# Kernel optimization log

Measured on AMD Instinct MI355X. Metric: run time of the kernel, lower is better.

Reference implementation:

```python
import jax, jax.numpy as jnp
import numpy as np

B, S, H, U = 32, 4096, 512, 512


def setup_inputs() -> dict:
    key = jax.random.key(0)
    ks = jax.random.split(key, 6)
    scale = 1.0 / np.sqrt(H)
    return {
        "query": jax.random.normal(ks[0], (B, H), dtype=jnp.float32),
        "values": jax.random.normal(ks[1], (B, S, H), dtype=jnp.float32),
        "W1": jax.random.normal(ks[2], (H, U), dtype=jnp.float32) * scale,
        "b1": jnp.zeros((U,), dtype=jnp.float32),
        "W2": jax.random.normal(ks[3], (H, U), dtype=jnp.float32) * scale,
        "b2": jnp.zeros((U,), dtype=jnp.float32),
        "va": jax.random.normal(ks[4], (U, 1), dtype=jnp.float32) * (1.0 / np.sqrt(U)),
        "bva": jnp.zeros((1,), dtype=jnp.float32),
    }


def reference(query, values, W1, b1, W2, b2, va, bva):
    # query: [B, H] -> [B, 1, U]; values: [B, S, H] -> [B, S, U]
    q_proj = jnp.einsum('bh,hu->bu', query, W1) + b1           # [B, U]
    v_proj = jnp.einsum('bsh,hu->bsu', values, W2) + b2        # [B, S, U]
    scores = jnp.einsum('bsu,uo->bso', jnp.tanh(q_proj[:, None, :] + v_proj), va) + bva  # [B, S, 1]
    attention_weights = jax.nn.softmax(scores, axis=1)         # [B, S, 1]
    context_vector = jnp.sum(attention_weights * values, axis=1)  # [B, H]
    return attention_weights, context_vector
```

## Files before the change

kernel.cpp:

```cpp
#include <hip/hip_runtime.h>
#include <hip/hip_bf16.h>
#include <stdint.h>

#define B_SZ 32
#define S_SZ 4096
#define H_SZ 512
#define U_SZ 512

typedef __attribute__((ext_vector_type(8)))  _Float16 half8;
typedef __attribute__((ext_vector_type(4)))  _Float16 half4_t;
typedef __attribute__((ext_vector_type(16))) float    floatx16;

__global__ __launch_bounds__(256) void qproj_kernel(
    const float* __restrict__ query, const float* __restrict__ W1,
    const float* __restrict__ b1, const float* __restrict__ b2,
    float* __restrict__ qpb2)
{
    const int b = blockIdx.x;
    const int u = blockIdx.y * 256 + threadIdx.x;
    float acc = b1[u] + b2[u];
    const float* q = query + b * H_SZ;
    for (int h = 0; h < H_SZ; ++h)
        acc += q[h] * W1[h * U_SZ + u];
    qpb2[b * U_SZ + u] = acc;
}

__global__ __launch_bounds__(256) void w2swizzle_kernel(
    const float* __restrict__ W2, _Float16* __restrict__ W2s)
{
    const int i = blockIdx.x * 256 + threadIdx.x;
    const int k = i >> 9;
    const int n = i & 511;
    const int idx = (k >> 4) * 8192 + ((k >> 3) & 1) * 4096 + n * 8 + (k & 7);
    W2s[idx] = (_Float16)W2[i];
}

__global__ __launch_bounds__(256, 2) void scores_kernel(
    const float* __restrict__ values, const _Float16* __restrict__ W2s,
    const float* __restrict__ qpb2, const float* __restrict__ va,
    const float* __restrict__ bva, float* __restrict__ scores)
{
    __shared__ __align__(16) _Float16 A_lds[1024];
    __shared__ __align__(16) _Float16 B_lds[8192];
    __shared__ float sc[64 * 33];

    const int t    = threadIdx.x;
    const int lane = t & 63;
    const int w    = t >> 6;
    const int l31  = lane & 31;
    const int kh   = lane >> 5;
    const int m0   = blockIdx.x * 64;
    const int b    = m0 >> 12;

    const float* Arow = values + (size_t)m0 * H_SZ;

    floatx16 acc[2][4];
#pragma unroll
    for (int s = 0; s < 2; ++s)
#pragma unroll
        for (int nt = 0; nt < 4; ++nt) acc[s][nt] = (floatx16)(0.0f);

    const int sm = t >> 2;
    const int kq = t & 3;
    const int aw = ((kq >> 1) * 64 + sm) * 8 + (kq & 1) * 4;

    const uint4* Wsrc = reinterpret_cast<const uint4*>(W2s);
    uint4* Bl4 = reinterpret_cast<uint4*>(B_lds);

    for (int kb = 0; kb < 32; ++kb) {
        __syncthreads();
        float4 av = *reinterpret_cast<const float4*>(Arow + sm * H_SZ + kb * 16 + kq * 4);
        half4_t ah;
        ah.x = (_Float16)av.x; ah.y = (_Float16)av.y;
        ah.z = (_Float16)av.z; ah.w = (_Float16)av.w;
        *reinterpret_cast<half4_t*>(&A_lds[aw]) = ah;
#pragma unroll
        for (int i = 0; i < 4; ++i)
            Bl4[t * 4 + i] = Wsrc[kb * 1024 + t * 4 + i];
        __syncthreads();

        half8 a0 = *reinterpret_cast<const half8*>(&A_lds[kh * 512 + l31 * 8]);
        half8 a1 = *reinterpret_cast<const half8*>(&A_lds[kh * 512 + 256 + l31 * 8]);
#pragma unroll
        for (int nt = 0; nt < 4; ++nt) {
            half8 bf = *reinterpret_cast<const half8*>(
                &B_lds[kh * 4096 + ((w * 4 + nt) * 32 + l31) * 8]);
            acc[0][nt] = __builtin_amdgcn_mfma_f32_32x32x16_f16(a0, bf, acc[0][nt], 0, 0, 0);
            acc[1][nt] = __builtin_amdgcn_mfma_f32_32x32x16_f16(a1, bf, acc[1][nt], 0, 0, 0);
        }
    }

    float qv[4], vv[4];
#pragma unroll
    for (int nt = 0; nt < 4; ++nt) {
        int n = w * 128 + nt * 32 + l31;
        qv[nt] = qpb2[b * U_SZ + n];
        vv[nt] = va[n];
    }
    __syncthreads();
    for (int i = t; i < 64 * 33; i += 256) sc[i] = 0.0f;
    __syncthreads();
#pragma unroll
    for (int s = 0; s < 2; ++s) {
#pragma unroll
        for (int r = 0; r < 16; ++r) {
            float p = 0.0f;
#pragma unroll
            for (int nt = 0; nt < 4; ++nt) {
                float x = acc[s][nt][r] + qv[nt];
                float e = __expf(2.0f * x);
                p += (1.0f - 2.0f / (e + 1.0f)) * vv[nt];
            }
            int ml = s * 32 + (r & 3) + 8 * (r >> 2) + 4 * kh;
            atomicAdd(&sc[ml * 33 + l31], p);
        }
    }
    __syncthreads();
    if (t < 64) {
        float sum = *bva;
#pragma unroll
        for (int c = 0; c < 32; ++c) sum += sc[t * 33 + c];
        scores[m0 + t] = sum;
    }
}

__global__ __launch_bounds__(1024) void softmax_kernel(
    const float* __restrict__ scores, float* __restrict__ out)
{
    __shared__ float red[16];
    __shared__ float s_max, s_sum;
    const int b = blockIdx.x;
    const int t = threadIdx.x;

    float4 v = *reinterpret_cast<const float4*>(scores + b * S_SZ + t * 4);
    float m = fmaxf(fmaxf(v.x, v.y), fmaxf(v.z, v.w));
#pragma unroll
    for (int o = 32; o > 0; o >>= 1) m = fmaxf(m, __shfl_xor(m, o));
    if ((t & 63) == 0) red[t >> 6] = m;
    __syncthreads();
    if (t == 0) {
        float mm = red[0];
        for (int i = 1; i < 16; ++i) mm = fmaxf(mm, red[i]);
        s_max = mm;
    }
    __syncthreads();
    float mm = s_max;
    float4 e;
    e.x = __expf(v.x - mm); e.y = __expf(v.y - mm);
    e.z = __expf(v.z - mm); e.w = __expf(v.w - mm);
    float s = e.x + e.y + e.z + e.w;
#pragma unroll
    for (int o = 32; o > 0; o >>= 1) s += __shfl_xor(s, o);
    if ((t & 63) == 0) red[t >> 6] = s;
    __syncthreads();
    if (t == 0) {
        float ss = 0.0f;
        for (int i = 0; i < 16; ++i) ss += red[i];
        s_sum = ss;
    }
    __syncthreads();
    float rinv = 1.0f / s_sum;
    float4 wv;
    wv.x = e.x * rinv; wv.y = e.y * rinv; wv.z = e.z * rinv; wv.w = e.w * rinv;
    *reinterpret_cast<float4*>(out + b * S_SZ + t * 4) = wv;

    if (t < 512) out[B_SZ * S_SZ + b * 512 + t] = 0.0f;
}

__global__ __launch_bounds__(256) void context_kernel(
    const float* __restrict__ values, const float* __restrict__ wts,
    float* __restrict__ ctx)
{
    __shared__ float wl[512];
    __shared__ __align__(16) float part[4][64][4];
    const int ss = blockIdx.x;
    const int hc = blockIdx.y;
    const int b  = blockIdx.z;
    const int t  = threadIdx.x;
    const int l = t & 63, g = t >> 6;

    if (t < 128)
        *reinterpret_cast<float4*>(&wl[t * 4]) =
            *reinterpret_cast<const float4*>(wts + b * S_SZ + ss * 512 + t * 4);
    __syncthreads();

    const int h = hc * 256 + l * 4;
    const float* vp = values + ((size_t)(b * S_SZ + ss * 512 + g * 128)) * H_SZ + h;
    float4 a = {0.f, 0.f, 0.f, 0.f};
    for (int i = 0; i < 128; ++i) {
        float wv = wl[g * 128 + i];
        float4 v = *reinterpret_cast<const float4*>(vp + (size_t)i * H_SZ);
        a.x += wv * v.x; a.y += wv * v.y; a.z += wv * v.z; a.w += wv * v.w;
    }
    *reinterpret_cast<float4*>(&part[g][l][0]) = a;
    __syncthreads();
    if (t < 64) {
        float4 sacc = *reinterpret_cast<float4*>(&part[0][t][0]);
#pragma unroll
        for (int gg = 1; gg < 4; ++gg) {
            float4 p = *reinterpret_cast<float4*>(&part[gg][t][0]);
            sacc.x += p.x; sacc.y += p.y; sacc.z += p.z; sacc.w += p.w;
        }
        int hh = hc * 256 + t * 4;
        atomicAdd(&ctx[b * H_SZ + hh + 0], sacc.x);
        atomicAdd(&ctx[b * H_SZ + hh + 1], sacc.y);
        atomicAdd(&ctx[b * H_SZ + hh + 2], sacc.z);
        atomicAdd(&ctx[b * H_SZ + hh + 3], sacc.w);
    }
}

extern "C" void kernel_launch(void* const* d_in, const int* in_sizes, int n_in,
                              void* d_out, int out_size, void* d_ws, size_t ws_size,
                              hipStream_t stream) {
    const float* query  = (const float*)d_in[0];
    const float* values = (const float*)d_in[1];
    const float* W1     = (const float*)d_in[2];
    const float* b1     = (const float*)d_in[3];
    const float* W2     = (const float*)d_in[4];
    const float* b2     = (const float*)d_in[5];
    const float* va     = (const float*)d_in[6];
    const float* bva    = (const float*)d_in[7];
    float* out = (float*)d_out;

    char* ws = (char*)d_ws;
    float*    qpb2   = (float*)ws;
    _Float16* W2s    = (_Float16*)(ws + 65536);
    float*    scores = (float*)(ws + 65536 + 524288);

    qproj_kernel<<<dim3(32, 2), 256, 0, stream>>>(query, W1, b1, b2, qpb2);
    w2swizzle_kernel<<<1024, 256, 0, stream>>>(W2, W2s);
    scores_kernel<<<2048, 256, 0, stream>>>(values, W2s, qpb2, va, bva, scores);
    softmax_kernel<<<32, 1024, 0, stream>>>(scores, out);
    context_kernel<<<dim3(8, 2, 32), 256, 0, stream>>>(values, out, out + B_SZ * S_SZ);
}
```

Baseline: 577.8 us.

## Rewrite scores GEMM with async double-buffered LDS and fuse softmax into context

```diff
diff --git a/kernel.cpp b/kernel.cpp
--- a/kernel.cpp
+++ b/kernel.cpp
@@ -7,32 +7,42 @@
 #define H_SZ 512
 #define U_SZ 512
 
-typedef __attribute__((ext_vector_type(8)))  _Float16 half8;
-typedef __attribute__((ext_vector_type(4)))  _Float16 half4_t;
-typedef __attribute__((ext_vector_type(16))) float    floatx16;
+typedef __attribute__((ext_vector_type(8))) _Float16 half8;
+typedef __attribute__((ext_vector_type(4))) float floatx4;
+
+__device__ __forceinline__ void async_copy16(const void* g, void* l) {
+    __builtin_amdgcn_global_load_lds(
+        (const __attribute__((address_space(1))) void*)g,
+        (__attribute__((address_space(3))) void*)l, 16, 0, 0);
+}
+
+__global__ __launch_bounds__(256) void prep_kernel(
+    const float* __restrict__ W2, _Float16* __restrict__ W2s,
+    float* __restrict__ qpb2, float* __restrict__ ctx)
+{
+    const int t = threadIdx.x;
+    const int bid = blockIdx.x;
+    const int i = bid * 256 + t;
+    const int k = i >> 9, n = i & 511;
+    W2s[(k >> 5) * 16384 + ((k >> 3) & 3) * 4096 + n * 8 + (k & 7)] =
+        (_Float16)W2[i];
+    if (bid < 64) qpb2[i] = 0.0f;
+    else if (bid < 128) ctx[(bid - 64) * 256 + t] = 0.0f;
+}
 
 __global__ __launch_bounds__(256) void qproj_kernel(
     const float* __restrict__ query, const float* __restrict__ W1,
     const float* __restrict__ b1, const float* __restrict__ b2,
     float* __restrict__ qpb2)
 {
-    const int b = blockIdx.x;
-    const int u = blockIdx.y * 256 + threadIdx.x;
-    float acc = b1[u] + b2[u];
-    const float* q = query + b * H_SZ;
-    for (int h = 0; h < H_SZ; ++h)
-        acc += q[h] * W1[h * U_SZ + u];
-    qpb2[b * U_SZ + u] = acc;
-}
-
-__global__ __launch_bounds__(256) void w2swizzle_kernel(
-    const float* __restrict__ W2, _Float16* __restrict__ W2s)
-{
-    const int i = blockIdx.x * 256 + threadIdx.x;
-    const int k = i >> 9;
-    const int n = i & 511;
-    const int idx = (k >> 4) * 8192 + ((k >> 3) & 1) * 4096 + n * 8 + (k & 7);
-    W2s[idx] = (_Float16)W2[i];
+    const int b = blockIdx.x, uc = blockIdx.y, ks = blockIdx.z;
+    const int u = uc * 256 + threadIdx.x;
+    float acc = (ks == 0) ? (b1[u] + b2[u]) : 0.0f;
+    const float* q  = query + b * H_SZ + ks * 128;
+    const float* Wp = W1 + (size_t)(ks * 128) * U_SZ + u;
+    for (int k = 0; k < 128; ++k)
+        acc = fmaf(q[k], Wp[(size_t)k * U_SZ], acc);
+    atomicAdd(&qpb2[b * U_SZ + u], acc);
 }
 
 __global__ __launch_bounds__(256, 2) void scores_kernel(
@@ -40,99 +50,125 @@
     const float* __restrict__ qpb2, const float* __restrict__ va,
     const float* __restrict__ bva, float* __restrict__ scores)
 {
-    __shared__ __align__(16) _Float16 A_lds[1024];
-    __shared__ __align__(16) _Float16 B_lds[8192];
-    __shared__ float sc[64 * 33];
-
-    const int t    = threadIdx.x;
-    const int lane = t & 63;
-    const int w    = t >> 6;
-    const int l31  = lane & 31;
-    const int kh   = lane >> 5;
-    const int m0   = blockIdx.x * 64;
-    const int b    = m0 >> 12;
-
-    const float* Arow = values + (size_t)m0 * H_SZ;
-
-    floatx16 acc[2][4];
-#pragma unroll
-    for (int s = 0; s < 2; ++s)
-#pragma unroll
-        for (int nt = 0; nt < 4; ++nt) acc[s][nt] = (floatx16)(0.0f);
-
-    const int sm = t >> 2;
-    const int kq = t & 3;
-    const int aw = ((kq >> 1) * 64 + sm) * 8 + (kq & 1) * 4;
-
-    const uint4* Wsrc = reinterpret_cast<const uint4*>(W2s);
-    uint4* Bl4 = reinterpret_cast<uint4*>(B_lds);
-
-    for (int kb = 0; kb < 32; ++kb) {
+    __shared__ __align__(16) char smem[65536];
+
+    const int t  = threadIdx.x;
+    const int w  = t >> 6;
+    const int l  = t & 63;
+    const int c  = l & 15;
+    const int g4 = l >> 4;
+    const int m0 = blockIdx.x * 64;
+    const int b  = m0 >> 12;
+
+    const float* Abase = values + (size_t)m0 * H_SZ;
+
+    floatx4 acc[4][8];
+#pragma unroll
+    for (int mt = 0; mt < 4; ++mt)
+#pragma unroll
+        for (int nt = 0; nt < 8; ++nt) acc[mt][nt] = (floatx4)(0.0f);
+
+    {
+        const char* src = (const char*)W2s;
+#pragma unroll
+        for (int i = 0; i < 8; ++i)
+            async_copy16(src + (i * 256 + t) * 16, smem + (i * 256 + t) * 16);
+    }
+    float4 Apre[4][2];
+    {
+        const int ko = g4 * 8;
+#pragma unroll
+        for (int mt = 0; mt < 4; ++mt) {
+            const float* ap = Abase + (size_t)(mt * 16 + c) * H_SZ + ko;
+            Apre[mt][0] = *(const float4*)(ap);
+            Apre[mt][1] = *(const float4*)(ap + 4);
+        }
+    }
+    __syncthreads();
+
+    for (int kb = 0; kb < 16; ++kb) {
+        const int cur = kb & 1;
+        half8 af[4];
+#pragma unroll
+        for (int mt = 0; mt < 4; ++mt) {
+            half8 a;
+            a[0] = (_Float16)Apre[mt][0].x; a[1] = (_Float16)Apre[mt][0].y;
+            a[2] = (_Float16)Apre[mt][0].z; a[3] = (_Float16)Apre[mt][0].w;
+            a[4] = (_Float16)Apre[mt][1].x; a[5] = (_Float16)Apre[mt][1].y;
+            a[6] = (_Float16)Apre[mt][1].z; a[7] = (_Float16)Apre[mt][1].w;
+            af[mt] = a;
+        }
+        if (kb < 15) {
+            const int ko = (kb + 1) * 32 + g4 * 8;
+#pragma unroll
+            for (int mt = 0; mt < 4; ++mt) {
+                const float* ap = Abase + (size_t)(mt * 16 + c) * H_SZ + ko;
+                Apre[mt][0] = *(const float4*)(ap);
+                Apre[mt][1] = *(const float4*)(ap + 4);
+            }
+            const char* src = (const char*)W2s + (size_t)(kb + 1) * 32768;
+            char* dst = smem + (cur ^ 1) * 32768;
+#pragma unroll
+            for (int i = 0; i < 8; ++i)
+                async_copy16(src + (i * 256 + t) * 16, dst + (i * 256 + t) * 16);
+        }
+        const _Float16* Bc = (const _Float16*)(smem + cur * 32768);
+        half8 bf[8];
+#pragma unroll
+        for (int nt = 0; nt < 8; ++nt)
+            bf[nt] = *(const half8*)(Bc + g4 * 4096 + (w * 128 + nt * 16 + c) * 8);
+#pragma unroll
+        for (int mt = 0; mt < 4; ++mt)
+#pragma unroll
+            for (int nt = 0; nt < 8; ++nt)
+                acc[mt][nt] = __builtin_amdgcn_mfma_f32_16x16x32_f16(
+                    af[mt], bf[nt], acc[mt][nt], 0, 0, 0);
         __syncthreads();
-        float4 av = *reinterpret_cast<const float4*>(Arow + sm * H_SZ + kb * 16 + kq * 4);
-        half4_t ah;
-        ah.x = (_Float16)av.x; ah.y = (_Float16)av.y;
-        ah.z = (_Float16)av.z; ah.w = (_Float16)av.w;
-        *reinterpret_cast<half4_t*>(&A_lds[aw]) = ah;
-#pragma unroll
-        for (int i = 0; i < 4; ++i)
-            Bl4[t * 4 + i] = Wsrc[kb * 1024 + t * 4 + i];
-        __syncthreads();
-
-        half8 a0 = *reinterpret_cast<const half8*>(&A_lds[kh * 512 + l31 * 8]);
-        half8 a1 = *reinterpret_cast<const half8*>(&A_lds[kh * 512 + 256 + l31 * 8]);
-#pragma unroll
-        for (int nt = 0; nt < 4; ++nt) {
-            half8 bf = *reinterpret_cast<const half8*>(
-                &B_lds[kh * 4096 + ((w * 4 + nt) * 32 + l31) * 8]);
-            acc[0][nt] = __builtin_amdgcn_mfma_f32_32x32x16_f16(a0, bf, acc[0][nt], 0, 0, 0);
-            acc[1][nt] = __builtin_amdgcn_mfma_f32_32x32x16_f16(a1, bf, acc[1][nt], 0, 0, 0);
-        }
-    }
-
-    float qv[4], vv[4];
-#pragma unroll
-    for (int nt = 0; nt < 4; ++nt) {
-        int n = w * 128 + nt * 32 + l31;
-        qv[nt] = qpb2[b * U_SZ + n];
-        vv[nt] = va[n];
-    }
-    __syncthreads();
-    for (int i = t; i < 64 * 33; i += 256) sc[i] = 0.0f;
-    __syncthreads();
-#pragma unroll
-    for (int s = 0; s < 2; ++s) {
-#pragma unroll
-        for (int r = 0; r < 16; ++r) {
+    }
+
+    float qv2[8], vv[8], vv2[8];
+#pragma unroll
+    for (int nt = 0; nt < 8; ++nt) {
+        const int n = w * 128 + nt * 16 + c;
+        const float q = qpb2[b * U_SZ + n];
+        const float v = va[n];
+        qv2[nt] = 2.0f * q;
+        vv[nt] = v;
+        vv2[nt] = 2.0f * v;
+    }
+    float* red = (float*)smem;
+#pragma unroll
+    for (int mt = 0; mt < 4; ++mt) {
+#pragma unroll
+        for (int r = 0; r < 4; ++r) {
             float p = 0.0f;
 #pragma unroll
-            for (int nt = 0; nt < 4; ++nt) {
-                float x = acc[s][nt][r] + qv[nt];
-                float e = __expf(2.0f * x);
-                p += (1.0f - 2.0f / (e + 1.0f)) * vv[nt];
+            for (int nt = 0; nt < 8; ++nt) {
+                const float ex = __expf(fmaf(acc[mt][nt][r], 2.0f, qv2[nt]));
+                const float rc = __builtin_amdgcn_rcpf(ex + 1.0f);
+                p = fmaf(-vv2[nt], rc, p + vv[nt]);
             }
-            int ml = s * 32 + (r & 3) + 8 * (r >> 2) + 4 * kh;
-            atomicAdd(&sc[ml * 33 + l31], p);
-        }
-    }
-    __syncthreads();
-    if (t < 64) {
-        float sum = *bva;
-#pragma unroll
-        for (int c = 0; c < 32; ++c) sum += sc[t * 33 + c];
-        scores[m0 + t] = sum;
-    }
-}
-
-__global__ __launch_bounds__(1024) void softmax_kernel(
-    const float* __restrict__ scores, float* __restrict__ out)
+            p += __shfl_xor(p, 1);
+            p += __shfl_xor(p, 2);
+            p += __shfl_xor(p, 4);
+            p += __shfl_xor(p, 8);
+            if (c == 0) red[(mt * 16 + g4 * 4 + r) * 4 + w] = p;
+        }
+    }
+    __syncthreads();
+    if (t < 64)
+        scores[m0 + t] = *bva + red[t * 4 + 0] + red[t * 4 + 1] +
+                         red[t * 4 + 2] + red[t * 4 + 3];
+}
+
+__global__ __launch_bounds__(1024) void sredux_kernel(
+    const float* __restrict__ scores, float* __restrict__ ML)
 {
     __shared__ float red[16];
-    __shared__ float s_max, s_sum;
+    __shared__ float s_max;
     const int b = blockIdx.x;
     const int t = threadIdx.x;
-
-    float4 v = *reinterpret_cast<const float4*>(scores + b * S_SZ + t * 4);
+    float4 v = *(const float4*)(scores + b * S_SZ + t * 4);
     float m = fmaxf(fmaxf(v.x, v.y), fmaxf(v.z, v.w));
 #pragma unroll
     for (int o = 32; o > 0; o >>= 1) m = fmaxf(m, __shfl_xor(m, o));
@@ -144,11 +180,9 @@
         s_max = mm;
     }
     __syncthreads();
-    float mm = s_max;
-    float4 e;
-    e.x = __expf(v.x - mm); e.y = __expf(v.y - mm);
-    e.z = __expf(v.z - mm); e.w = __expf(v.w - mm);
-    float s = e.x + e.y + e.z + e.w;
+    const float mm = s_max;
+    float s = __expf(v.x - mm) + __expf(v.y - mm) +
+              __expf(v.z - mm) + __expf(v.w - mm);
 #pragma unroll
     for (int o = 32; o > 0; o >>= 1) s += __shfl_xor(s, o);
     if ((t & 63) == 0) red[t >> 6] = s;
@@ -156,56 +190,57 @@
     if (t == 0) {
         float ss = 0.0f;
         for (int i = 0; i < 16; ++i) ss += red[i];
-        s_sum = ss;
-    }
-    __syncthreads();
-    float rinv = 1.0f / s_sum;
-    float4 wv;
-    wv.x = e.x * rinv; wv.y = e.y * rinv; wv.z = e.z * rinv; wv.w = e.w * rinv;
-    *reinterpret_cast<float4*>(out + b * S_SZ + t * 4) = wv;
-
-    if (t < 512) out[B_SZ * S_SZ + b * 512 + t] = 0.0f;
+        ML[b * 2] = mm;
+        ML[b * 2 + 1] = ss;
+    }
 }
 
 __global__ __launch_bounds__(256) void context_kernel(
-    const float* __restrict__ values, const float* __restrict__ wts,
-    float* __restrict__ ctx)
-{
-    __shared__ float wl[512];
+    const float* __restrict__ values, const float* __restrict__ scores,
+    const float* __restrict__ ML, float* __restrict__ out)
+{
+    __shared__ float wl[256];
     __shared__ __align__(16) float part[4][64][4];
-    const int ss = blockIdx.x;
-    const int hc = blockIdx.y;
-    const int b  = blockIdx.z;
-    const int t  = threadIdx.x;
+    const int ss = blockIdx.x, hc = blockIdx.y, b = blockIdx.z;
+    const int t = threadIdx.x;
+    const float M = ML[b * 2];
+    const float rL = 1.0f / ML[b * 2 + 1];
+    const int s = ss * 256 + t;
+    const float wv = __expf(scores[b * S_SZ + s] - M) * rL;
+    wl[t] = wv;
+    if (hc == 0) out[b * S_SZ + s] = wv;
+    __syncthreads();
+
     const int l = t & 63, g = t >> 6;
-
-    if (t < 128)
-        *reinterpret_cast<float4*>(&wl[t * 4]) =
-            *reinterpret_cast<const float4*>(wts + b * S_SZ + ss * 512 + t * 4);
-    __syncthreads();
-
     const int h = hc * 256 + l * 4;
-    const float* vp = values + ((size_t)(b * S_SZ + ss * 512 + g * 128)) * H_SZ + h;
-    float4 a = {0.f, 0.f, 0.f, 0.f};
-    for (int i = 0; i < 128; ++i) {
-        float wv = wl[g * 128 + i];
-        float4 v = *reinterpret_cast<const float4*>(vp + (size_t)i * H_SZ);
-        a.x += wv * v.x; a.y += wv * v.y; a.z += wv * v.z; a.w += wv * v.w;
-    }
-    *reinterpret_cast<float4*>(&part[g][l][0]) = a;
+    const float* vp = values + ((size_t)b * S_SZ + ss * 256 + g * 64) * H_SZ + h;
+    float4 a0 = {0.f, 0.f, 0.f, 0.f}, a1 = {0.f, 0.f, 0.f, 0.f};
+    for (int i = 0; i < 64; i += 2) {
+        const float w0 = wl[g * 64 + i];
+        const float w1 = wl[g * 64 + i + 1];
+        float4 v0 = *(const float4*)(vp + (size_t)i * H_SZ);
+        float4 v1 = *(const float4*)(vp + (size_t)(i + 1) * H_SZ);
+        a0.x = fmaf(w0, v0.x, a0.x); a0.y = fmaf(w0, v0.y, a0.y);
+        a0.z = fmaf(w0, v0.z, a0.z); a0.w = fmaf(w0, v0.w, a0.w);
+        a1.x = fmaf(w1, v1.x, a1.x); a1.y = fmaf(w1, v1.y, a1.y);
+        a1.z = fmaf(w1, v1.z, a1.z); a1.w = fmaf(w1, v1.w, a1.w);
+    }
+    a0.x += a1.x; a0.y += a1.y; a0.z += a1.z; a0.w += a1.w;
+    *(float4*)&part[g][l][0] = a0;
     __syncthreads();
     if (t < 64) {
-        float4 sacc = *reinterpret_cast<float4*>(&part[0][t][0]);
+        float4 sa = *(float4*)&part[0][t][0];
 #pragma unroll
         for (int gg = 1; gg < 4; ++gg) {
-            float4 p = *reinterpret_cast<float4*>(&part[gg][t][0]);
-            sacc.x += p.x; sacc.y += p.y; sacc.z += p.z; sacc.w += p.w;
-        }
-        int hh = hc * 256 + t * 4;
-        atomicAdd(&ctx[b * H_SZ + hh + 0], sacc.x);
-        atomicAdd(&ctx[b * H_SZ + hh + 1], sacc.y);
-        atomicAdd(&ctx[b * H_SZ + hh + 2], sacc.z);
-        atomicAdd(&ctx[b * H_SZ + hh + 3], sacc.w);
+            float4 p = *(float4*)&part[gg][t][0];
+            sa.x += p.x; sa.y += p.y; sa.z += p.z; sa.w += p.w;
+        }
+        float* ctx = out + B_SZ * S_SZ;
+        const int hh = hc * 256 + t * 4;
+        atomicAdd(&ctx[b * H_SZ + hh + 0], sa.x);
+        atomicAdd(&ctx[b * H_SZ + hh + 1], sa.y);
+        atomicAdd(&ctx[b * H_SZ + hh + 2], sa.z);
+        atomicAdd(&ctx[b * H_SZ + hh + 3], sa.w);
     }
 }
 
@@ -226,10 +261,13 @@
     float*    qpb2   = (float*)ws;
     _Float16* W2s    = (_Float16*)(ws + 65536);
     float*    scores = (float*)(ws + 65536 + 524288);
-
-    qproj_kernel<<<dim3(32, 2), 256, 0, stream>>>(query, W1, b1, b2, qpb2);
-    w2swizzle_kernel<<<1024, 256, 0, stream>>>(W2, W2s);
+    float*    ML     = (float*)(ws + 65536 + 524288 + 524288);
+
+    float* ctx = out + B_SZ * S_SZ;
+
+    prep_kernel<<<1024, 256, 0, stream>>>(W2, W2s, qpb2, ctx);
+    qproj_kernel<<<dim3(32, 2, 4), 256, 0, stream>>>(query, W1, b1, b2, qpb2);
     scores_kernel<<<2048, 256, 0, stream>>>(values, W2s, qpb2, va, bva, scores);
-    softmax_kernel<<<32, 1024, 0, stream>>>(scores, out);
-    context_kernel<<<dim3(8, 2, 32), 256, 0, stream>>>(values, out, out + B_SZ * S_SZ);
-}
+    sredux_kernel<<<32, 1024, 0, stream>>>(scores, ML);
+    context_kernel<<<dim3(16, 2, 32), 256, 0, stream>>>(values, scores, ML, out);
+}
```

Result: faster. 545.9 us (-5.5%).
